# Optimization experiments

Hardware: AMD Instinct MI355X
Metric: run time of the kernel (lower is better)

The kernel has to match this reference:

```python
import jax, jax.numpy as jnp
import numpy as np


def _pair_indices(num_fields):
    i_idx, j_idx = np.triu_indices(num_fields, k=1)  # row-major (i, then j>i) matches the torch loop order
    return jnp.asarray(i_idx), jnp.asarray(j_idx)


def setup_inputs() -> dict:
    key = jax.random.key(0)
    k1, k2 = jax.random.split(key)
    B, F, D = 2048, 40, 64
    P = F * (F - 1) // 2  # 780 pairs
    x = jax.random.normal(k1, (B, F, D), dtype=jnp.float32)
    W = jax.random.normal(k2, (P, D, D), dtype=jnp.float32) * (1.0 / np.sqrt(D))
    return {"x": x, "W": W}


def reference(x, W):
    # x: [B, F, D], W: [P, D, D] with P = F*(F-1)//2 (field_interaction)
    B, F, D = x.shape
    i_idx, j_idx = _pair_indices(F)
    vi = x[:, i_idx, :]  # [B, P, D]
    vj = x[:, j_idx, :]  # [B, P, D]
    # vi @ W_p @ vj for every pair p, vectorized: [B, P]
    viW = jnp.einsum("bpd,pde->bpe", vi, W)
    out = jnp.einsum("bpe,bpe->bp", viW, vj)
    return out
```

## Files before the change

kernel.cpp:

```cpp
#include <hip/hip_runtime.h>
#include <hip/hip_bf16.h>

typedef float f32x4 __attribute__((ext_vector_type(4)));
typedef __bf16 bf16x8 __attribute__((ext_vector_type(8)));
typedef unsigned short ushort8 __attribute__((ext_vector_type(8)));
typedef unsigned short u16x4 __attribute__((ext_vector_type(4)));

constexpr int kB = 2048;
constexpr int kF = 40;
constexpr int kD = 64;
constexpr int kP = 780;
constexpr int kFD = kF * kD;

constexpr size_t X_BF_ELEMS = (size_t)kB * kFD;
constexpr size_t X_BF_BYTES = X_BF_ELEMS * 2;
constexpr size_t W2_VEC_CNT = (size_t)kP * 512;
constexpr size_t W2_BYTES   = W2_VEC_CNT * 16;
constexpr size_t WS_NEEDED  = X_BF_BYTES + W2_BYTES;

constexpr int XCONV_BLOCKS = (int)(X_BF_ELEMS / 8 / 256);
constexpr int PRE_BLOCKS = XCONV_BLOCKS + kP;

__device__ __forceinline__ unsigned short f2bf_bits(float f) {
  unsigned u = __builtin_bit_cast(unsigned, f);
  u += 0x7FFFu + ((u >> 16) & 1u);
  return (unsigned short)(u >> 16);
}
__device__ __forceinline__ float bf2f(unsigned short u) {
  return __builtin_bit_cast(float, (unsigned)u << 16);
}

__global__ __launch_bounds__(256) void bilinear_prepass(
    const float* __restrict__ x, const float* __restrict__ W,
    unsigned short* __restrict__ x_bf, ushort8* __restrict__ W2) {
  __shared__ unsigned short wl[4096];
  const int blk = blockIdx.x;
  const int tid = threadIdx.x;
  if (blk < XCONV_BLOCKS) {
    const size_t i = ((size_t)blk * 256 + tid) * 8;
    f32x4 v0 = *(const f32x4*)(x + i);
    f32x4 v1 = *(const f32x4*)(x + i + 4);
    ushort8 o;
#pragma unroll
    for (int t = 0; t < 4; ++t) {
      o[t] = f2bf_bits(v0[t]);
      o[t + 4] = f2bf_bits(v1[t]);
    }
    *(ushort8*)(x_bf + i) = o;
  } else {
    const int p = blk - XCONV_BLOCKS;
    const float* wp = W + (size_t)p * (kD * kD);
#pragma unroll
    for (int k = 0; k < 4; ++k) {
      int i4 = tid + (k << 8);
      f32x4 v = *(const f32x4*)(wp + i4 * 4);
      u16x4 o;
#pragma unroll
      for (int t = 0; t < 4; ++t) o[t] = f2bf_bits(v[t]);
      *(u16x4*)(wl + i4 * 4) = o;
    }
    __syncthreads();
#pragma unroll
    for (int r = 0; r < 2; ++r) {
      int v = tid + (r << 8);
      int frag = v >> 6, lane = v & 63;
      int kk = frag >> 2, nb = frag & 3;
      int lo = lane & 15, h2 = lane >> 4;
      ushort8 o;
#pragma unroll
      for (int t = 0; t < 8; ++t)
        o[t] = wl[(kk * 32 + h2 * 8 + t) * 64 + nb * 16 + lo];
      W2[(size_t)p * 512 + v] = o;
    }
  }
}

template <int NRG, int RSB, int JOFFB, bool CROSS>
__device__ __forceinline__ void pair_loop(
    const unsigned char* smem, const ushort8* __restrict__ W2,
    float* __restrict__ out, int fa, int fb_, int row0,
    int wv, int lo, int hi, int lane) {
  const int NP = CROSS ? 100 : 45;
  int prev_ii = -1;
  ushort8 af[NRG][2];

  int ii, jj;
  {
    int q = wv;
    if constexpr (CROSS) { ii = q / 10; jj = q - ii * 10; }
    else { int s = 0; ii = 0; while (s + 9 - ii <= q) { s += 9 - ii; ++ii; } jj = ii + 1 + (q - s); }
  }
  ushort8 wnx[8];
  {
    int gi = fa + ii, gj = fb_ + jj;
    size_t wb = (size_t)(gi * kF - ((gi * (gi + 1)) >> 1) + gj - gi - 1) * 512;
#pragma unroll
    for (int f = 0; f < 8; ++f) wnx[f] = W2[wb + f * 64 + lane];
  }

  for (int q = wv; q < NP; q += 8) {
    const int cii = ii, cjj = jj;
    ushort8 wc[8];
#pragma unroll
    for (int f = 0; f < 8; ++f) wc[f] = wnx[f];

    int qn = q + 8;
    if (qn < NP) {
      if constexpr (CROSS) { ii = qn / 10; jj = qn - ii * 10; }
      else { int s = 0; ii = 0; while (s + 9 - ii <= qn) { s += 9 - ii; ++ii; } jj = ii + 1 + (qn - s); }
      int gi = fa + ii, gj = fb_ + jj;
      size_t wb = (size_t)(gi * kF - ((gi * (gi + 1)) >> 1) + gj - gi - 1) * 512;
#pragma unroll
      for (int f = 0; f < 8; ++f) wnx[f] = W2[wb + f * 64 + lane];
    }

    if (cii != prev_ii) {
      prev_ii = cii;
#pragma unroll
      for (int rg = 0; rg < NRG; ++rg) {
        int row_l = rg * 16 + lo;
        int sw = (row_l & 7) << 4;
#pragma unroll
        for (int kk = 0; kk < 2; ++kk)
          af[rg][kk] = *(const ushort8*)(
              smem + row_l * RSB + ((cii * 128 + kk * 64 + hi * 16) ^ sw));
      }
    }

    const int gi = fa + cii, gj = fb_ + cjj;
    const int p = gi * kF - ((gi * (gi + 1)) >> 1) + gj - gi - 1;

#pragma unroll
    for (int rg = 0; rg < NRG; ++rg) {
      int row_l = rg * 16 + lo;
      int sw = (row_l & 7) << 4;
      u16x4 xj[4];
#pragma unroll
      for (int nb = 0; nb < 4; ++nb)
        xj[nb] = *(const u16x4*)(
            smem + row_l * RSB + ((JOFFB + cjj * 128 + nb * 32 + hi * 8) ^ sw));

      f32x4 acc[4];
#pragma unroll
      for (int nb = 0; nb < 4; ++nb) acc[nb] = f32x4{0.f, 0.f, 0.f, 0.f};
#pragma unroll
      for (int kk = 0; kk < 2; ++kk)
#pragma unroll
        for (int nb = 0; nb < 4; ++nb)
          acc[nb] = __builtin_amdgcn_mfma_f32_16x16x32_bf16(
              __builtin_bit_cast(bf16x8, wc[kk * 4 + nb]),
              __builtin_bit_cast(bf16x8, af[rg][kk]), acc[nb], 0, 0, 0);

      float sm[4];
#pragma unroll
      for (int nb = 0; nb < 4; ++nb)
        sm[nb] = fmaf(acc[nb][3], bf2f(xj[nb][3]),
                 fmaf(acc[nb][2], bf2f(xj[nb][2]),
                 fmaf(acc[nb][1], bf2f(xj[nb][1]),
                      acc[nb][0] * bf2f(xj[nb][0]))));
      float sum = (sm[0] + sm[1]) + (sm[2] + sm[3]);
      sum += __shfl_xor(sum, 16, 64);
      sum += __shfl_xor(sum, 32, 64);
      if (hi == 0) out[(size_t)(row0 + row_l) * kP + p] = sum;
    }
  }
}

__global__ __launch_bounds__(512) void bilinear_main4(
    const unsigned short* __restrict__ x_bf, const ushort8* __restrict__ W2,
    float* __restrict__ out) {
  __shared__ __align__(16) unsigned char smem[163840];
  const int gid = blockIdx.x;
  const int item = ((gid & 7) << 5) + (gid >> 3);
  const int tid = threadIdx.x;
  const int lane = tid & 63;
  const int wv = tid >> 6;
  const int lo = lane & 15;
  const int hi = lane >> 4;

  if (item < 192) {
    const int cls = item >> 5;
    const int tile = item & 31;
    int a, b;
    if (cls < 3)      { a = 0; b = cls + 1; }
    else if (cls < 5) { a = 1; b = cls - 1; }
    else              { a = 2; b = 3; }
    const int fa = a * 10, fb_ = b * 10;
    const int row0 = tile * 64;
#pragma unroll
    for (int k = 0; k < 20; ++k) {
      int c = tid + (k << 9);
      int rowc = c / 160;
      int rem = c - rowc * 160;
      int half = rem >= 80;
      int off16 = half ? rem - 80 : rem;
      const unsigned short* src = x_bf + (size_t)(row0 + rowc) * kFD
                                  + (half ? fb_ : fa) * 64 + off16 * 8;
      ushort8 v = *(const ushort8*)src;
      int dst = rowc * 2560 + ((half * 1280 + off16 * 16) ^ ((rowc & 7) << 4));
      *(ushort8*)(smem + dst) = v;
    }
    __syncthreads();
    pair_loop<4, 2560, 1280, true>(smem, W2, out, fa, fb_, row0, wv, lo, hi, lane);
  } else {
    const int d = (item - 192) >> 4;
    const int tile = (item - 192) & 15;
    const int fa = d * 10;
    const int row0 = tile * 128;
#pragma unroll
    for (int k = 0; k < 20; ++k) {
      int c = tid + (k << 9);
      int rowc = c / 80;
      int off16 = c - rowc * 80;
      const unsigned short* src = x_bf + (size_t)(row0 + rowc) * kFD + fa * 64 + off16 * 8;
      ushort8 v = *(const ushort8*)src;
      *(ushort8*)(smem + rowc * 1280 + ((off16 * 16) ^ ((rowc & 7) << 4))) = v;
    }
    __syncthreads();
    pair_loop<8, 1280, 0, false>(smem, W2, out, fa, fa, row0, wv, lo, hi, lane);
  }
}

__global__ __launch_bounds__(256) void bilinear_fb(
    const float* __restrict__ x, const float* __restrict__ W,
    float* __restrict__ out) {
  const int gid = blockIdx.x;
  const int item = (gid & 7) * 390 + (gid >> 3);
  const int p = item >> 2;
  const int btile = item & 3;
  int i_f = 0, s = 0;
  while (s + (kF - 1 - i_f) <= p) { s += kF - 1 - i_f; ++i_f; }
  const int j_f = i_f + 1 + (p - s);
  const int lane = threadIdx.x & 63;
  const int wave = threadIdx.x >> 6;
  const int lo = lane & 15;
  const int hi = lane >> 4;
  const float* wp = W + (size_t)p * (kD * kD);
  bf16x8 bfrag[2][4];
#pragma unroll
  for (int kk = 0; kk < 2; ++kk)
#pragma unroll
    for (int nb = 0; nb < 4; ++nb) {
      ushort8 tmp;
#pragma unroll
      for (int t = 0; t < 8; ++t)
        tmp[t] = f2bf_bits(wp[(kk * 32 + hi * 8 + t) * kD + nb * 16 + lo]);
      bfrag[kk][nb] = __builtin_bit_cast(bf16x8, tmp);
    }
  const int b0 = btile * 512;
  for (int pass = 0; pass < 8; ++pass) {
    const int rb = b0 + pass * 64 + wave * 16;
    const float* xi = x + (size_t)(rb + lo) * kFD + i_f * kD;
    bf16x8 afrag[2];
#pragma unroll
    for (int kk = 0; kk < 2; ++kk) {
      f32x4 v0 = *(const f32x4*)(xi + kk * 32 + hi * 8);
      f32x4 v1 = *(const f32x4*)(xi + kk * 32 + hi * 8 + 4);
      ushort8 tmp;
#pragma unroll
      for (int t = 0; t < 4; ++t) {
        tmp[t] = f2bf_bits(v0[t]);
        tmp[t + 4] = f2bf_bits(v1[t]);
      }
      afrag[kk] = __builtin_bit_cast(bf16x8, tmp);
    }
    f32x4 acc[4];
#pragma unroll
    for (int nb = 0; nb < 4; ++nb) acc[nb] = f32x4{0.f, 0.f, 0.f, 0.f};
#pragma unroll
    for (int kk = 0; kk < 2; ++kk)
#pragma unroll
      for (int nb = 0; nb < 4; ++nb)
        acc[nb] = __builtin_amdgcn_mfma_f32_16x16x32_bf16(afrag[kk], bfrag[kk][nb],
                                                          acc[nb], 0, 0, 0);
#pragma unroll
    for (int q = 0; q < 4; ++q) {
      const int row = rb + hi * 4 + q;
      const float* xj = x + (size_t)row * kFD + j_f * kD + lo;
      float sum = 0.f;
#pragma unroll
      for (int nb = 0; nb < 4; ++nb) sum += acc[nb][q] * xj[nb * 16];
      sum += __shfl_xor(sum, 1, 64);
      sum += __shfl_xor(sum, 2, 64);
      sum += __shfl_xor(sum, 4, 64);
      sum += __shfl_xor(sum, 8, 64);
      if (lo == 0) out[(size_t)row * kP + p] = sum;
    }
  }
}

extern "C" void kernel_launch(void* const* d_in, const int* in_sizes, int n_in,
                              void* d_out, int out_size, void* d_ws, size_t ws_size,
                              hipStream_t stream) {
  const float* x = (const float*)d_in[0];
  const float* W = (const float*)d_in[1];
  float* out = (float*)d_out;
  if (ws_size >= WS_NEEDED) {
    unsigned short* x_bf = (unsigned short*)d_ws;
    ushort8* W2 = (ushort8*)((char*)d_ws + X_BF_BYTES);
    hipLaunchKernelGGL(bilinear_prepass, dim3(PRE_BLOCKS), dim3(256), 0, stream,
                       x, W, x_bf, W2);
    hipLaunchKernelGGL(bilinear_main4, dim3(256), dim3(512), 0, stream,
                       x_bf, W2, out);
  } else {
    hipLaunchKernelGGL(bilinear_fb, dim3(3120), dim3(256), 0, stream, x, W, out);
  }
}
```

Before: 104.4 us.

## Fuse weight prepass into main kernel via cooperative grid sync, convert x inline

The separate prepass kernel is replaced by a single cooperative kernel. Each block first converts and reorders a slice of the W pairs into the bf16 fragment layout, then the whole grid synchronises before the main pair loop. The x tile is now converted from fp32 to bf16 while it is loaded into shared memory, so the x_bf staging buffer and its global round trip go away. This saves a kernel launch and roughly 10 MB of intermediate traffic, at the cost of a grid-wide barrier, cooperative launch overhead, and reading fp32 x, which is twice the bytes of the bf16 copy.

```diff
diff --git a/kernel.cpp b/kernel.cpp
--- a/kernel.cpp
+++ b/kernel.cpp
@@ -1,5 +1,8 @@
 #include <hip/hip_runtime.h>
 #include <hip/hip_bf16.h>
+#include <hip/hip_cooperative_groups.h>
+
+namespace cg = cooperative_groups;
 
 typedef float f32x4 __attribute__((ext_vector_type(4)));
 typedef __bf16 bf16x8 __attribute__((ext_vector_type(8)));
@@ -12,14 +15,8 @@
 constexpr int kP = 780;
 constexpr int kFD = kF * kD;
 
-constexpr size_t X_BF_ELEMS = (size_t)kB * kFD;
-constexpr size_t X_BF_BYTES = X_BF_ELEMS * 2;
-constexpr size_t W2_VEC_CNT = (size_t)kP * 512;
-constexpr size_t W2_BYTES   = W2_VEC_CNT * 16;
-constexpr size_t WS_NEEDED  = X_BF_BYTES + W2_BYTES;
-
-constexpr int XCONV_BLOCKS = (int)(X_BF_ELEMS / 8 / 256);
-constexpr int PRE_BLOCKS = XCONV_BLOCKS + kP;
+constexpr size_t W2_BYTES  = (size_t)kP * 512 * 16;
+constexpr size_t WS_NEEDED = W2_BYTES;
 
 __device__ __forceinline__ unsigned short f2bf_bits(float f) {
   unsigned u = __builtin_bit_cast(unsigned, f);
@@ -28,51 +25,6 @@
 }
 __device__ __forceinline__ float bf2f(unsigned short u) {
   return __builtin_bit_cast(float, (unsigned)u << 16);
-}
-
-__global__ __launch_bounds__(256) void bilinear_prepass(
-    const float* __restrict__ x, const float* __restrict__ W,
-    unsigned short* __restrict__ x_bf, ushort8* __restrict__ W2) {
-  __shared__ unsigned short wl[4096];
-  const int blk = blockIdx.x;
-  const int tid = threadIdx.x;
-  if (blk < XCONV_BLOCKS) {
-    const size_t i = ((size_t)blk * 256 + tid) * 8;
-    f32x4 v0 = *(const f32x4*)(x + i);
-    f32x4 v1 = *(const f32x4*)(x + i + 4);
-    ushort8 o;
-#pragma unroll
-    for (int t = 0; t < 4; ++t) {
-      o[t] = f2bf_bits(v0[t]);
-      o[t + 4] = f2bf_bits(v1[t]);
-    }
-    *(ushort8*)(x_bf + i) = o;
-  } else {
-    const int p = blk - XCONV_BLOCKS;
-    const float* wp = W + (size_t)p * (kD * kD);
-#pragma unroll
-    for (int k = 0; k < 4; ++k) {
-      int i4 = tid + (k << 8);
-      f32x4 v = *(const f32x4*)(wp + i4 * 4);
-      u16x4 o;
-#pragma unroll
-      for (int t = 0; t < 4; ++t) o[t] = f2bf_bits(v[t]);
-      *(u16x4*)(wl + i4 * 4) = o;
-    }
-    __syncthreads();
-#pragma unroll
-    for (int r = 0; r < 2; ++r) {
-      int v = tid + (r << 8);
-      int frag = v >> 6, lane = v & 63;
-      int kk = frag >> 2, nb = frag & 3;
-      int lo = lane & 15, h2 = lane >> 4;
-      ushort8 o;
-#pragma unroll
-      for (int t = 0; t < 8; ++t)
-        o[t] = wl[(kk * 32 + h2 * 8 + t) * 64 + nb * 16 + lo];
-      W2[(size_t)p * 512 + v] = o;
-    }
-  }
 }
 
 template <int NRG, int RSB, int JOFFB, bool CROSS>
@@ -166,27 +118,71 @@
   }
 }
 
-__global__ __launch_bounds__(512) void bilinear_main4(
-    const unsigned short* __restrict__ x_bf, const ushort8* __restrict__ W2,
-    float* __restrict__ out) {
+__global__ __launch_bounds__(512) void bilinear_coop(
+    const float* __restrict__ x, const float* __restrict__ W,
+    ushort8* __restrict__ W2, float* __restrict__ out) {
   __shared__ __align__(16) unsigned char smem[163840];
   const int gid = blockIdx.x;
-  const int item = ((gid & 7) << 5) + (gid >> 3);
   const int tid = threadIdx.x;
   const int lane = tid & 63;
   const int wv = tid >> 6;
   const int lo = lane & 15;
   const int hi = lane >> 4;
-
+  const int item = ((gid & 7) << 5) + (gid >> 3);
+
+  int fa, fb_, row0, tile;
+  bool cross;
   if (item < 192) {
-    const int cls = item >> 5;
-    const int tile = item & 31;
+    cross = true;
+    int cls = item >> 5; tile = item & 31;
     int a, b;
     if (cls < 3)      { a = 0; b = cls + 1; }
     else if (cls < 5) { a = 1; b = cls - 1; }
     else              { a = 2; b = 3; }
-    const int fa = a * 10, fb_ = b * 10;
-    const int row0 = tile * 64;
+    fa = a * 10; fb_ = b * 10; row0 = tile * 64;
+  } else {
+    cross = false;
+    int d = (item - 192) >> 4; tile = (item - 192) & 15;
+    fa = d * 10; fb_ = fa; row0 = tile * 128;
+  }
+
+  unsigned short* wl = (unsigned short*)smem;
+  const int NP   = cross ? 100 : 45;
+  const int STEP = cross ? 32 : 16;
+  for (int q = tile; q < NP; q += STEP) {
+    int ii, jj;
+    if (cross) { ii = q / 10; jj = q - ii * 10; }
+    else { int s = 0; ii = 0; while (s + 9 - ii <= q) { s += 9 - ii; ++ii; } jj = ii + 1 + (q - s); }
+    const int gi = fa + ii, gj = fb_ + jj;
+    const int p = gi * kF - ((gi * (gi + 1)) >> 1) + gj - gi - 1;
+    const float* wp = W + (size_t)p * (kD * kD);
+#pragma unroll
+    for (int k = 0; k < 2; ++k) {
+      int i4 = tid + (k << 9);
+      f32x4 v = *(const f32x4*)(wp + i4 * 4);
+      u16x4 o;
+#pragma unroll
+      for (int t = 0; t < 4; ++t) o[t] = f2bf_bits(v[t]);
+      *(u16x4*)(wl + i4 * 4) = o;
+    }
+    __syncthreads();
+    {
+      int v = tid;
+      int frag = v >> 6, ln = v & 63;
+      int kk = frag >> 2, nb = frag & 3;
+      int l2 = ln & 15, h2 = ln >> 4;
+      ushort8 o;
+#pragma unroll
+      for (int t = 0; t < 8; ++t)
+        o[t] = wl[(kk * 32 + h2 * 8 + t) * 64 + nb * 16 + l2];
+      W2[(size_t)p * 512 + v] = o;
+    }
+    __syncthreads();
+  }
+  __threadfence();
+  cg::this_grid().sync();
+
+  if (cross) {
 #pragma unroll
     for (int k = 0; k < 20; ++k) {
       int c = tid + (k << 9);
@@ -194,27 +190,31 @@
       int rem = c - rowc * 160;
       int half = rem >= 80;
       int off16 = half ? rem - 80 : rem;
-      const unsigned short* src = x_bf + (size_t)(row0 + rowc) * kFD
-                                  + (half ? fb_ : fa) * 64 + off16 * 8;
-      ushort8 v = *(const ushort8*)src;
+      const float* src = x + (size_t)(row0 + rowc) * kFD
+                         + (half ? fb_ : fa) * 64 + off16 * 8;
+      f32x4 v0 = *(const f32x4*)src;
+      f32x4 v1 = *(const f32x4*)(src + 4);
+      ushort8 o;
+#pragma unroll
+      for (int t = 0; t < 4; ++t) { o[t] = f2bf_bits(v0[t]); o[t + 4] = f2bf_bits(v1[t]); }
       int dst = rowc * 2560 + ((half * 1280 + off16 * 16) ^ ((rowc & 7) << 4));
-      *(ushort8*)(smem + dst) = v;
+      *(ushort8*)(smem + dst) = o;
     }
     __syncthreads();
     pair_loop<4, 2560, 1280, true>(smem, W2, out, fa, fb_, row0, wv, lo, hi, lane);
   } else {
-    const int d = (item - 192) >> 4;
-    const int tile = (item - 192) & 15;
-    const int fa = d * 10;
-    const int row0 = tile * 128;
 #pragma unroll
     for (int k = 0; k < 20; ++k) {
       int c = tid + (k << 9);
       int rowc = c / 80;
       int off16 = c - rowc * 80;
-      const unsigned short* src = x_bf + (size_t)(row0 + rowc) * kFD + fa * 64 + off16 * 8;
-      ushort8 v = *(const ushort8*)src;
-      *(ushort8*)(smem + rowc * 1280 + ((off16 * 16) ^ ((rowc & 7) << 4))) = v;
+      const float* src = x + (size_t)(row0 + rowc) * kFD + fa * 64 + off16 * 8;
+      f32x4 v0 = *(const f32x4*)src;
+      f32x4 v1 = *(const f32x4*)(src + 4);
+      ushort8 o;
+#pragma unroll
+      for (int t = 0; t < 4; ++t) { o[t] = f2bf_bits(v0[t]); o[t + 4] = f2bf_bits(v1[t]); }
+      *(ushort8*)(smem + rowc * 1280 + ((off16 * 16) ^ ((rowc & 7) << 4))) = o;
     }
     __syncthreads();
     pair_loop<8, 1280, 0, false>(smem, W2, out, fa, fa, row0, wv, lo, hi, lane);
@@ -296,12 +296,10 @@
   const float* W = (const float*)d_in[1];
   float* out = (float*)d_out;
   if (ws_size >= WS_NEEDED) {
-    unsigned short* x_bf = (unsigned short*)d_ws;
-    ushort8* W2 = (ushort8*)((char*)d_ws + X_BF_BYTES);
-    hipLaunchKernelGGL(bilinear_prepass, dim3(PRE_BLOCKS), dim3(256), 0, stream,
-                       x, W, x_bf, W2);
-    hipLaunchKernelGGL(bilinear_main4, dim3(256), dim3(512), 0, stream,
-                       x_bf, W2, out);
+    ushort8* W2 = (ushort8*)d_ws;
+    void* args[] = {(void*)&x, (void*)&W, (void*)&W2, (void*)&out};
+    hipLaunchCooperativeKernel((void*)bilinear_coop, dim3(256), dim3(512),
+                               args, 0, stream);
   } else {
     hipLaunchKernelGGL(bilinear_fb, dim3(3120), dim3(256), 0, stream, x, W, out);
   }
```

Result: slower. 176.2 us (+68.8%).
